# Kernel optimization log

Hardware: AMD Instinct MI355X
Metric: run time of the kernel (lower is better)

Reference implementation:

```python
import jax, jax.numpy as jnp
import numpy as np

K_HIDDEN = 512
N_POS = 24
N_COLOR = 6
EPS = 1e-5


def setup_inputs() -> dict:
    key = jax.random.key(0)
    k1, k2 = jax.random.split(key)
    B = 1024
    x = jax.random.normal(k1, (B, N_POS, N_COLOR * K_HIDDEN), dtype=jnp.float32)
    # kaiming-uniform-ish scale for the (k_out, k_in, 2) weight
    fan_in = K_HIDDEN * 2
    bound = float(np.sqrt(6.0 / fan_in))
    conv_weight = jax.random.uniform(k2, (K_HIDDEN, K_HIDDEN, 2), dtype=jnp.float32,
                                     minval=-bound, maxval=bound)
    conv_bias = jnp.zeros((K_HIDDEN,), dtype=jnp.float32)
    norm_weight = jnp.ones((K_HIDDEN,), dtype=jnp.float32)
    norm_bias = jnp.zeros((K_HIDDEN,), dtype=jnp.float32)
    return {"x": x, "conv_weight": conv_weight, "conv_bias": conv_bias,
            "norm_weight": norm_weight, "norm_bias": norm_bias}


def _color_layernorm(x, gamma, beta):
    # x: (B, 24, 6*k); normalize over the full channel axis, affine tied per block of 6
    mean = jnp.mean(x, axis=-1, keepdims=True)
    var = jnp.mean(jnp.square(x - mean), axis=-1, keepdims=True)  # unbiased=False
    xn = (x - mean) * jax.lax.rsqrt(var + EPS)
    xn = xn.reshape(*x.shape[:-1], K_HIDDEN, N_COLOR)
    xn = xn * gamma[:, None] + beta[:, None]
    return xn.reshape(x.shape)


def _color_conv(x, weight, bias):
    # x: (B, 24, 6*k) -> (B, 24, k, 6)
    B = x.shape[0]
    xr = x.reshape(B, N_POS, K_HIDDEN, N_COLOR)
    alpha = weight[:, :, 0] - weight[:, :, 1]   # (k_out, k_in)
    beta_w = weight[:, :, 1]                    # (k_out, k_in)
    term1 = jnp.einsum('bikd,ok->biod', xr, alpha)      # per-color linear
    x_sum = xr.sum(axis=3)                               # (B, 24, k_in)
    term2 = jnp.einsum('bik,ok->bio', x_sum, beta_w)     # color-sum linear
    out = term1 + term2[..., None] + bias[None, None, :, None]
    return out.reshape(B, N_POS, K_HIDDEN * N_COLOR)


def reference(x, conv_weight, conv_bias, norm_weight, norm_bias):
    h = _color_layernorm(x, norm_weight, norm_bias)
    h = _color_conv(h, conv_weight, conv_bias)
    return x + jax.nn.relu(h)
```

## Files before the change

### kernel.cpp

```cpp
#include <hip/hip_runtime.h>
#include <stdint.h>
#include <stddef.h>

#define KH   512
#define DF   3072
#define EPSF 1e-5f
#define PPB  8
#define ROWS 48
#define TSS  516

typedef __attribute__((ext_vector_type(4))) float f32x4;
typedef __attribute__((ext_vector_type(2))) float f32x2;
typedef __attribute__((ext_vector_type(8))) short bf16x8;

__device__ __forceinline__ unsigned short f2bf(float f) {
  union { float f; unsigned u; } c; c.f = f;
  unsigned u = c.u;
  u += 0x7fffu + ((u >> 16) & 1u);
  return (unsigned short)(u >> 16);
}
__device__ __forceinline__ unsigned short f2bf_trunc(float f) {
  union { float f; unsigned u; } c; c.f = f;
  return (unsigned short)(c.u >> 16);
}
__device__ __forceinline__ float bf2f(unsigned short u) {
  union { unsigned u; float f; } c; c.u = ((unsigned)u) << 16;
  return c.f;
}

__global__ __launch_bounds__(256) void prep_w(const float* __restrict__ cw,
                                              const float* __restrict__ cb,
                                              const float* __restrict__ nw,
                                              const float* __restrict__ nb,
                                              unsigned char* __restrict__ wbt,
                                              float* __restrict__ c12) {
  const int o = blockIdx.x;
  const int t = threadIdx.x;
  const int wn = o >> 6, nn = (o >> 4) & 3, co = o & 15;
  float c1 = 0.f, c2 = 0.f;
  for (int k = t; k < KH; k += 256) {
    float w0 = cw[o * 1024 + 2 * k];
    float w1 = cw[o * 1024 + 2 * k + 1];
    float a  = w0 - w1;
    float g  = nw[k], b = nb[k];
    int s = k >> 5, kin = k & 31, h = kin >> 3, e = kin & 7;
    size_t base = (size_t)(((wn * 16 + s) * 4 + nn)) * 1024 + (h * 16 + co) * 16 + e * 2;
    *(unsigned short*)(wbt + base)          = f2bf(a * g);
    *(unsigned short*)(wbt + base + 524288) = f2bf(w1 * g);
    float tt = a + 6.f * w1;
    c1 += tt * b;
    c2 += tt * g;
  }
  #pragma unroll
  for (int off = 32; off >= 1; off >>= 1) {
    c1 += __shfl_xor(c1, off);
    c2 += __shfl_xor(c2, off);
  }
  __shared__ float s1[4], s2[4];
  int wid = t >> 6, lane = t & 63;
  if (lane == 0) { s1[wid] = c1; s2[wid] = c2; }
  __syncthreads();
  if (t == 0) {
    c12[o]      = s1[0] + s1[1] + s1[2] + s1[3] + cb[o];
    c12[KH + o] = s2[0] + s2[1] + s2[2] + s2[3];
  }
}

__global__ __launch_bounds__(512, 4) void fused_main(
    const float* __restrict__ x,
    const unsigned char* __restrict__ wbt,
    const float* __restrict__ c12,
    float* __restrict__ out)
{
  __shared__ unsigned char As[ROWS * 1024];
  __shared__ unsigned char Sx[PPB * 1024];
  __shared__ float Ts[PPB * TSS];
  __shared__ float st[PPB * 2];

  const int tid  = threadIdx.x;
  const int lane = tid & 63;
  const int wid  = tid >> 6;
  const int co   = lane & 15;
  const int h    = lane >> 4;
  const int rvb  = h << 2;
  const size_t r0 = (size_t)blockIdx.x * PPB;

  const unsigned char* wA = wbt + (size_t)wid * 65536;
  bf16x8 bvA[4], bvB[4];

  {
    const float* xr = x + (size_t)(r0 + wid) * DF + lane * 48;
    f32x4 q[12];
    #pragma unroll
    for (int i = 0; i < 12; i++) q[i] = *(const f32x4*)(xr + i * 4);

    #pragma unroll
    for (int n = 0; n < 4; n++)
      bvA[n] = *(const bf16x8*)(wA + n * 1024 + lane * 16);

    float vv[48];
    #pragma unroll
    for (int i = 0; i < 12; i++) {
      vv[4 * i] = q[i].x; vv[4 * i + 1] = q[i].y;
      vv[4 * i + 2] = q[i].z; vv[4 * i + 3] = q[i].w;
    }
    float s = 0.f, sq = 0.f;
    #pragma unroll
    for (int i = 0; i < 48; i++) { s += vv[i]; sq += vv[i] * vv[i]; }
    #pragma unroll
    for (int off = 32; off >= 1; off >>= 1) {
      s  += __shfl_xor(s,  off);
      sq += __shfl_xor(sq, off);
    }
    float mean = s * (1.f / 3072.f);
    float var  = sq * (1.f / 3072.f) - mean * mean;
    float rstd = rsqrtf(var + EPSF);
    if (lane == 0) { st[2 * wid] = mean; st[2 * wid + 1] = rstd; }

    #pragma unroll
    for (int d = 0; d < 6; d++) {
      int row = wid * 6 + d;
      bf16x8 v;
      #pragma unroll
      for (int g = 0; g < 8; g++) v[g] = (short)f2bf_trunc(vv[g * 6 + d]);
      *(bf16x8*)(As + row * 1024 + ((lane ^ (row & 7)) << 4)) = v;
    }
    bf16x8 sv;
    #pragma unroll
    for (int g = 0; g < 8; g++) {
      float ss = vv[g * 6] + vv[g * 6 + 1] + vv[g * 6 + 2] +
                 vv[g * 6 + 3] + vv[g * 6 + 4] + vv[g * 6 + 5];
      sv[g] = (short)f2bf_trunc(ss);
    }
    *(bf16x8*)(Sx + wid * 1024 + ((lane ^ (wid & 7)) << 4)) = sv;
  }
  __syncthreads();

  f32x4 acc1[3][4];
  #pragma unroll
  for (int m = 0; m < 3; m++)
    #pragma unroll
    for (int n = 0; n < 4; n++) acc1[m][n] = (f32x4){0.f, 0.f, 0.f, 0.f};

  int arow[3], ar7[3];
  #pragma unroll
  for (int m = 0; m < 3; m++) {
    int row = m * 16 + co;
    arow[m] = row * 1024;  ar7[m] = row & 7;
  }

  {
    bf16x8 afA[3], afB[3];
    #pragma unroll
    for (int m = 0; m < 3; m++)
      afA[m] = *(const bf16x8*)(As + arow[m] + ((h ^ ar7[m]) << 4));

    #pragma unroll 1
    for (int s = 0; s < 16; s += 2) {
      {
        int g6 = (s + 1) * 4 + h;
        #pragma unroll
        for (int m = 0; m < 3; m++)
          afB[m] = *(const bf16x8*)(As + arow[m] + ((g6 ^ ar7[m]) << 4));
        const unsigned char* pn = wA + (size_t)(s + 1) * 4096;
        #pragma unroll
        for (int n = 0; n < 4; n++)
          bvB[n] = *(const bf16x8*)(pn + n * 1024 + lane * 16);
      }
      __builtin_amdgcn_s_setprio(1);
      #pragma unroll
      for (int m = 0; m < 3; m++)
        #pragma unroll
        for (int n = 0; n < 4; n++)
          acc1[m][n] = __builtin_amdgcn_mfma_f32_16x16x32_bf16(afA[m], bvA[n], acc1[m][n], 0, 0, 0);
      __builtin_amdgcn_s_setprio(0);
      if (s + 2 < 16) {
        int g6 = (s + 2) * 4 + h;
        #pragma unroll
        for (int m = 0; m < 3; m++)
          afA[m] = *(const bf16x8*)(As + arow[m] + ((g6 ^ ar7[m]) << 4));
        const unsigned char* pn2 = wA + (size_t)(s + 2) * 4096;
        #pragma unroll
        for (int n = 0; n < 4; n++)
          bvA[n] = *(const bf16x8*)(pn2 + n * 1024 + lane * 16);
      }
      __builtin_amdgcn_s_setprio(1);
      #pragma unroll
      for (int m = 0; m < 3; m++)
        #pragma unroll
        for (int n = 0; n < 4; n++)
          acc1[m][n] = __builtin_amdgcn_mfma_f32_16x16x32_bf16(afB[m], bvB[n], acc1[m][n], 0, 0, 0);
      __builtin_amdgcn_s_setprio(0);
    }
  }

  {
    f32x4 acc2[4];
    #pragma unroll
    for (int n = 0; n < 4; n++) acc2[n] = (f32x4){0.f, 0.f, 0.f, 0.f};
    const unsigned char* wB2 = wbt + 524288 + (size_t)wid * 65536;
    const int sxr = (co & 7);
    bf16x8 cA[4], cB[4];
    bf16x8 a2A, a2B;
    #pragma unroll
    for (int n = 0; n < 4; n++)
      cA[n] = *(const bf16x8*)(wB2 + n * 1024 + lane * 16);
    a2A = *(const bf16x8*)(Sx + sxr * 1024 + ((h ^ sxr) << 4));

    #pragma unroll 1
    for (int s = 0; s < 16; s += 2) {
      {
        int g6 = (s + 1) * 4 + h;
        a2B = *(const bf16x8*)(Sx + sxr * 1024 + ((g6 ^ sxr) << 4));
        const unsigned char* pn = wB2 + (size_t)(s + 1) * 4096;
        #pragma unroll
        for (int n = 0; n < 4; n++)
          cB[n] = *(const bf16x8*)(pn + n * 1024 + lane * 16);
      }
      __builtin_amdgcn_s_setprio(1);
      #pragma unroll
      for (int n = 0; n < 4; n++)
        acc2[n] = __builtin_amdgcn_mfma_f32_16x16x32_bf16(a2A, cA[n], acc2[n], 0, 0, 0);
      __builtin_amdgcn_s_setprio(0);
      if (s + 2 < 16) {
        int g6 = (s + 2) * 4 + h;
        a2A = *(const bf16x8*)(Sx + sxr * 1024 + ((g6 ^ sxr) << 4));
        const unsigned char* pn2 = wB2 + (size_t)(s + 2) * 4096;
        #pragma unroll
        for (int n = 0; n < 4; n++)
          cA[n] = *(const bf16x8*)(pn2 + n * 1024 + lane * 16);
      }
      __builtin_amdgcn_s_setprio(1);
      #pragma unroll
      for (int n = 0; n < 4; n++)
        acc2[n] = __builtin_amdgcn_mfma_f32_16x16x32_bf16(a2B, cB[n], acc2[n], 0, 0, 0);
      __builtin_amdgcn_s_setprio(0);
    }
    if (h < 2) {
      #pragma unroll
      for (int n = 0; n < 4; n++)
        #pragma unroll
        for (int v = 0; v < 4; v++)
          Ts[(rvb + v) * TSS + wid * 64 + n * 16 + co] = acc2[n][v];
    }
  }

  #pragma unroll
  for (int n = 0; n < 4; n++) {
    const int o = wid * 64 + n * 16 + co;
    const float C1 = c12[o];
    const float C2 = c12[KH + o];
    const int swzo = o >> 3;
    const int ob2 = (o & 7) * 2;
    #pragma unroll
    for (int m = 0; m < 3; m++) {
      int j0  = m * 16 + rvb;
      int pl0 = j0 / 6;
      int d0  = j0 - pl0 * 6;
      float mean0 = st[2 * pl0], rstd0 = st[2 * pl0 + 1];
      float t20   = Ts[pl0 * TSS + o];
      float cc0   = C1 - mean0 * rstd0 * C2;
      if (d0 < 3) {
        f32x4 ov;
        #pragma unroll
        for (int v = 0; v < 4; v++) {
          int j = j0 + v;
          unsigned short rx = *(const unsigned short*)(
              As + j * 1024 + ((swzo ^ (j & 7)) << 4) + ob2);
          ov[v] = bf2f(rx) + fmaxf(rstd0 * (acc1[m][n][v] + t20) + cc0, 0.f);
        }
        *(f32x4*)(out + (r0 + pl0) * DF + o * 6 + d0) = ov;
      } else {
        int pl1 = pl0 + 1;
        float mean1 = st[2 * pl1], rstd1 = st[2 * pl1 + 1];
        float t21   = Ts[pl1 * TSS + o];
        float cc1   = C1 - mean1 * rstd1 * C2;
        f32x2 o0, o1;
        #pragma unroll
        for (int v = 0; v < 2; v++) {
          int j = j0 + v;
          unsigned short rx = *(const unsigned short*)(
              As + j * 1024 + ((swzo ^ (j & 7)) << 4) + ob2);
          o0[v] = bf2f(rx) + fmaxf(rstd0 * (acc1[m][n][v] + t20) + cc0, 0.f);
        }
        #pragma unroll
        for (int v = 2; v < 4; v++) {
          int j = j0 + v;
          unsigned short rx = *(const unsigned short*)(
              As + j * 1024 + ((swzo ^ (j & 7)) << 4) + ob2);
          o1[v - 2] = bf2f(rx) + fmaxf(rstd1 * (acc1[m][n][v] + t21) + cc1, 0.f);
        }
        *(f32x2*)(out + (r0 + pl0) * DF + o * 6 + 4) = o0;
        *(f32x2*)(out + (r0 + pl1) * DF + o * 6)     = o1;
      }
    }
  }
}

extern "C" void kernel_launch(void* const* d_in, const int* in_sizes, int n_in,
                              void* d_out, int out_size, void* d_ws, size_t ws_size,
                              hipStream_t stream) {
  (void)n_in; (void)out_size; (void)ws_size;
  const float* x  = (const float*)d_in[0];
  const float* cw = (const float*)d_in[1];
  const float* cb = (const float*)d_in[2];
  const float* nw = (const float*)d_in[3];
  const float* nb = (const float*)d_in[4];
  float* out = (float*)d_out;

  unsigned char* wbt = (unsigned char*)d_ws;
  float* c12 = (float*)((char*)d_ws + (size_t)1024 * 1024);

  prep_w<<<512, 256, 0, stream>>>(cw, cb, nw, nb, wbt, c12);

  const int R = in_sizes[0] / DF;
  fused_main<<<R / PPB, 512, 0, stream>>>(x, wbt, c12, out);
}
```

Measured before the change: 234.1 us.

## Double rows per block with 16 waves sharing weight tiles

Each block now handles 16 positions (96 rows) with 1024 threads arranged as 2x8 waves. Waves in the same column share one weight slice, so each weight byte loaded from L2 serves twice as many rows. The colour-sum GEMM is split so each wave computes 32 output columns across all 16 positions. The change adds a barrier before the epilogue and raises LDS use per block, which may limit occupancy and register availability.

```diff
diff --git a/kernel.cpp b/kernel.cpp
--- a/kernel.cpp
+++ b/kernel.cpp
@@ -5,8 +5,8 @@
 #define KH   512
 #define DF   3072
 #define EPSF 1e-5f
-#define PPB  8
-#define ROWS 48
+#define PPB  16
+#define ROWS 96
 #define TSS  516
 
 typedef __attribute__((ext_vector_type(4))) float f32x4;
@@ -66,7 +66,7 @@
   }
 }
 
-__global__ __launch_bounds__(512, 4) void fused_main(
+__global__ __launch_bounds__(1024, 4) void fused_main(
     const float* __restrict__ x,
     const unsigned char* __restrict__ wbt,
     const float* __restrict__ c12,
@@ -80,12 +80,14 @@
   const int tid  = threadIdx.x;
   const int lane = tid & 63;
   const int wid  = tid >> 6;
+  const int wm   = wid >> 3;
+  const int wn   = wid & 7;
   const int co   = lane & 15;
   const int h    = lane >> 4;
   const int rvb  = h << 2;
   const size_t r0 = (size_t)blockIdx.x * PPB;
 
-  const unsigned char* wA = wbt + (size_t)wid * 65536;
+  const unsigned char* wA = wbt + (size_t)wn * 65536;
   bf16x8 bvA[4], bvB[4];
 
   {
@@ -145,7 +147,7 @@
   int arow[3], ar7[3];
   #pragma unroll
   for (int m = 0; m < 3; m++) {
-    int row = m * 16 + co;
+    int row = wm * 48 + m * 16 + co;
     arow[m] = row * 1024;  ar7[m] = row & 7;
   }
 
@@ -195,66 +197,62 @@
   }
 
   {
-    f32x4 acc2[4];
-    #pragma unroll
-    for (int n = 0; n < 4; n++) acc2[n] = (f32x4){0.f, 0.f, 0.f, 0.f};
-    const unsigned char* wB2 = wbt + 524288 + (size_t)wid * 65536;
-    const int sxr = (co & 7);
-    bf16x8 cA[4], cB[4];
+    f32x4 acc2[2];
+    acc2[0] = (f32x4){0.f, 0.f, 0.f, 0.f};
+    acc2[1] = (f32x4){0.f, 0.f, 0.f, 0.f};
+    const unsigned char* wB2 = wbt + 524288 + (size_t)(wid >> 1) * 65536
+                             + (size_t)(2 * (wid & 1)) * 1024 + (size_t)lane * 16;
+    const int sxr = co;
+    const int sx7 = sxr & 7;
+    bf16x8 cA[2], cB[2];
     bf16x8 a2A, a2B;
-    #pragma unroll
-    for (int n = 0; n < 4; n++)
-      cA[n] = *(const bf16x8*)(wB2 + n * 1024 + lane * 16);
-    a2A = *(const bf16x8*)(Sx + sxr * 1024 + ((h ^ sxr) << 4));
+    cA[0] = *(const bf16x8*)(wB2);
+    cA[1] = *(const bf16x8*)(wB2 + 1024);
+    a2A = *(const bf16x8*)(Sx + sxr * 1024 + ((h ^ sx7) << 4));
 
     #pragma unroll 1
     for (int s = 0; s < 16; s += 2) {
       {
         int g6 = (s + 1) * 4 + h;
-        a2B = *(const bf16x8*)(Sx + sxr * 1024 + ((g6 ^ sxr) << 4));
+        a2B = *(const bf16x8*)(Sx + sxr * 1024 + ((g6 ^ sx7) << 4));
         const unsigned char* pn = wB2 + (size_t)(s + 1) * 4096;
-        #pragma unroll
-        for (int n = 0; n < 4; n++)
-          cB[n] = *(const bf16x8*)(pn + n * 1024 + lane * 16);
+        cB[0] = *(const bf16x8*)(pn);
+        cB[1] = *(const bf16x8*)(pn + 1024);
       }
       __builtin_amdgcn_s_setprio(1);
-      #pragma unroll
-      for (int n = 0; n < 4; n++)
-        acc2[n] = __builtin_amdgcn_mfma_f32_16x16x32_bf16(a2A, cA[n], acc2[n], 0, 0, 0);
+      acc2[0] = __builtin_amdgcn_mfma_f32_16x16x32_bf16(a2A, cA[0], acc2[0], 0, 0, 0);
+      acc2[1] = __builtin_amdgcn_mfma_f32_16x16x32_bf16(a2A, cA[1], acc2[1], 0, 0, 0);
       __builtin_amdgcn_s_setprio(0);
       if (s + 2 < 16) {
         int g6 = (s + 2) * 4 + h;
-        a2A = *(const bf16x8*)(Sx + sxr * 1024 + ((g6 ^ sxr) << 4));
+        a2A = *(const bf16x8*)(Sx + sxr * 1024 + ((g6 ^ sx7) << 4));
         const unsigned char* pn2 = wB2 + (size_t)(s + 2) * 4096;
-        #pragma unroll
-        for (int n = 0; n < 4; n++)
-          cA[n] = *(const bf16x8*)(pn2 + n * 1024 + lane * 16);
+        cA[0] = *(const bf16x8*)(pn2);
+        cA[1] = *(const bf16x8*)(pn2 + 1024);
       }
       __builtin_amdgcn_s_setprio(1);
+      acc2[0] = __builtin_amdgcn_mfma_f32_16x16x32_bf16(a2B, cB[0], acc2[0], 0, 0, 0);
+      acc2[1] = __builtin_amdgcn_mfma_f32_16x16x32_bf16(a2B, cB[1], acc2[1], 0, 0, 0);
+      __builtin_amdgcn_s_setprio(0);
+    }
+    #pragma unroll
+    for (int n = 0; n < 2; n++)
       #pragma unroll
-      for (int n = 0; n < 4; n++)
-        acc2[n] = __builtin_amdgcn_mfma_f32_16x16x32_bf16(a2B, cB[n], acc2[n], 0, 0, 0);
-      __builtin_amdgcn_s_setprio(0);
-    }
-    if (h < 2) {
-      #pragma unroll
-      for (int n = 0; n < 4; n++)
-        #pragma unroll
-        for (int v = 0; v < 4; v++)
-          Ts[(rvb + v) * TSS + wid * 64 + n * 16 + co] = acc2[n][v];
-    }
-  }
+      for (int v = 0; v < 4; v++)
+        Ts[(rvb + v) * TSS + wid * 32 + n * 16 + co] = acc2[n][v];
+  }
+  __syncthreads();
 
   #pragma unroll
   for (int n = 0; n < 4; n++) {
-    const int o = wid * 64 + n * 16 + co;
+    const int o = wn * 64 + n * 16 + co;
     const float C1 = c12[o];
     const float C2 = c12[KH + o];
     const int swzo = o >> 3;
     const int ob2 = (o & 7) * 2;
     #pragma unroll
     for (int m = 0; m < 3; m++) {
-      int j0  = m * 16 + rvb;
+      int j0  = wm * 48 + m * 16 + rvb;
       int pl0 = j0 / 6;
       int d0  = j0 - pl0 * 6;
       float mean0 = st[2 * pl0], rstd0 = st[2 * pl0 + 1];
@@ -314,5 +312,5 @@
   prep_w<<<512, 256, 0, stream>>>(cw, cb, nw, nb, wbt, c12);
 
   const int R = in_sizes[0] / DF;
-  fused_main<<<R / PPB, 512, 0, stream>>>(x, wbt, c12, out);
-}
+  fused_main<<<R / PPB, 1024, 0, stream>>>(x, wbt, c12, out);
+}
```

New measurement: 240.5 us. 1.03x slower.

## Warp-specialize fused kernel into producer/consumer pipeline over double-buffered tiles

Applied to the files above, without the earlier changes.

Each block now has 16 waves and handles 12 consecutive 8-row tiles in a loop. Eight producer waves load x, compute LayerNorm statistics, fill the next tile's bf16 LDS buffers and write out the previous tile. Eight consumer waves run both MFMA GEMMs and write the residual result back into the LDS A buffer as bf16. The aim is to overlap global loads and stores with MFMA work and to cut the block count. The cost is only 8 compute waves per CU, a per-tile barrier, and a final output rounded to bf16 instead of fp32, which may affect accuracy.

```diff
diff --git a/kernel.cpp b/kernel.cpp
--- a/kernel.cpp
+++ b/kernel.cpp
@@ -7,10 +7,12 @@
 #define EPSF 1e-5f
 #define PPB  8
 #define ROWS 48
+#define NT   12
 #define TSS  516
+#define ABYTES (ROWS * 1024)
+#define SBYTES (PPB * 1024)
 
 typedef __attribute__((ext_vector_type(4))) float f32x4;
-typedef __attribute__((ext_vector_type(2))) float f32x2;
 typedef __attribute__((ext_vector_type(8))) short bf16x8;
 
 __device__ __forceinline__ unsigned short f2bf(float f) {
@@ -66,234 +68,261 @@
   }
 }
 
-__global__ __launch_bounds__(512, 4) void fused_main(
+__device__ __forceinline__ void stats_fill(const f32x4* q, unsigned char* Ab,
+                                           unsigned char* Sb, float* stb,
+                                           int pw, int lane) {
+  float vv[48];
+  #pragma unroll
+  for (int i = 0; i < 12; i++) {
+    vv[4*i] = q[i].x; vv[4*i+1] = q[i].y; vv[4*i+2] = q[i].z; vv[4*i+3] = q[i].w;
+  }
+  float s = 0.f, sq = 0.f;
+  #pragma unroll
+  for (int i = 0; i < 48; i++) { s += vv[i]; sq += vv[i] * vv[i]; }
+  #pragma unroll
+  for (int off = 32; off >= 1; off >>= 1) {
+    s  += __shfl_xor(s,  off);
+    sq += __shfl_xor(sq, off);
+  }
+  float mean = s * (1.f / 3072.f);
+  float var  = sq * (1.f / 3072.f) - mean * mean;
+  float rstd = rsqrtf(var + EPSF);
+  if (lane == 0) { stb[2 * pw] = mean; stb[2 * pw + 1] = rstd; }
+  #pragma unroll
+  for (int d = 0; d < 6; d++) {
+    int row = pw * 6 + d;
+    bf16x8 v;
+    #pragma unroll
+    for (int g = 0; g < 8; g++) v[g] = (short)f2bf_trunc(vv[g * 6 + d]);
+    *(bf16x8*)(Ab + row * 1024 + ((lane ^ (row & 7)) << 4)) = v;
+  }
+  bf16x8 sv;
+  #pragma unroll
+  for (int g = 0; g < 8; g++) {
+    float ss = vv[g*6] + vv[g*6+1] + vv[g*6+2] + vv[g*6+3] + vv[g*6+4] + vv[g*6+5];
+    sv[g] = (short)f2bf_trunc(ss);
+  }
+  *(bf16x8*)(Sb + pw * 1024 + ((lane ^ (pw & 7)) << 4)) = sv;
+}
+
+__device__ __forceinline__ void store_out_panel(const unsigned char* Ab,
+                                                float* ob, int pw, int lane) {
+  #pragma unroll
+  for (int jj = 0; jj < 12; jj++) {
+    int c0 = jj * 256 + lane * 4;
+    int o0 = c0 / 6;
+    int d0 = c0 - o0 * 6;
+    f32x4 ov;
+    #pragma unroll
+    for (int e = 0; e < 4; e++) {
+      int d = d0 + e, o = o0;
+      if (d >= 6) { d -= 6; o += 1; }
+      int row  = pw * 6 + d;
+      int byte = row * 1024 + ((((o >> 3) ^ (row & 7)) << 4)) + (o & 7) * 2;
+      ov[e] = bf2f(*(const unsigned short*)(Ab + byte));
+    }
+    *(f32x4*)(ob + c0) = ov;
+  }
+}
+
+__global__ __launch_bounds__(1024, 4) void fused_main(
     const float* __restrict__ x,
     const unsigned char* __restrict__ wbt,
     const float* __restrict__ c12,
     float* __restrict__ out)
 {
-  __shared__ unsigned char As[ROWS * 1024];
-  __shared__ unsigned char Sx[PPB * 1024];
+  __shared__ unsigned char As_[2 * ABYTES];
+  __shared__ unsigned char Sx_[2 * SBYTES];
   __shared__ float Ts[PPB * TSS];
-  __shared__ float st[PPB * 2];
+  __shared__ float st[2][PPB * 2];
 
   const int tid  = threadIdx.x;
   const int lane = tid & 63;
   const int wid  = tid >> 6;
+  const int pw   = wid & 7;
+  const bool isProd = wid >= 8;
   const int co   = lane & 15;
   const int h    = lane >> 4;
   const int rvb  = h << 2;
-  const size_t r0 = (size_t)blockIdx.x * PPB;
-
-  const unsigned char* wA = wbt + (size_t)wid * 65536;
-  bf16x8 bvA[4], bvB[4];
-
-  {
-    const float* xr = x + (size_t)(r0 + wid) * DF + lane * 48;
+  const size_t tile0 = (size_t)blockIdx.x * NT;
+
+  if (isProd) {
     f32x4 q[12];
+    const float* xr = x + (tile0 * PPB + pw) * DF + lane * 48;
     #pragma unroll
     for (int i = 0; i < 12; i++) q[i] = *(const f32x4*)(xr + i * 4);
-
-    #pragma unroll
-    for (int n = 0; n < 4; n++)
-      bvA[n] = *(const bf16x8*)(wA + n * 1024 + lane * 16);
-
-    float vv[48];
-    #pragma unroll
-    for (int i = 0; i < 12; i++) {
-      vv[4 * i] = q[i].x; vv[4 * i + 1] = q[i].y;
-      vv[4 * i + 2] = q[i].z; vv[4 * i + 3] = q[i].w;
-    }
-    float s = 0.f, sq = 0.f;
-    #pragma unroll
-    for (int i = 0; i < 48; i++) { s += vv[i]; sq += vv[i] * vv[i]; }
-    #pragma unroll
-    for (int off = 32; off >= 1; off >>= 1) {
-      s  += __shfl_xor(s,  off);
-      sq += __shfl_xor(sq, off);
-    }
-    float mean = s * (1.f / 3072.f);
-    float var  = sq * (1.f / 3072.f) - mean * mean;
-    float rstd = rsqrtf(var + EPSF);
-    if (lane == 0) { st[2 * wid] = mean; st[2 * wid + 1] = rstd; }
-
-    #pragma unroll
-    for (int d = 0; d < 6; d++) {
-      int row = wid * 6 + d;
-      bf16x8 v;
-      #pragma unroll
-      for (int g = 0; g < 8; g++) v[g] = (short)f2bf_trunc(vv[g * 6 + d]);
-      *(bf16x8*)(As + row * 1024 + ((lane ^ (row & 7)) << 4)) = v;
-    }
-    bf16x8 sv;
-    #pragma unroll
-    for (int g = 0; g < 8; g++) {
-      float ss = vv[g * 6] + vv[g * 6 + 1] + vv[g * 6 + 2] +
-                 vv[g * 6 + 3] + vv[g * 6 + 4] + vv[g * 6 + 5];
-      sv[g] = (short)f2bf_trunc(ss);
-    }
-    *(bf16x8*)(Sx + wid * 1024 + ((lane ^ (wid & 7)) << 4)) = sv;
+    stats_fill(q, As_, Sx_, st[0], pw, lane);
   }
   __syncthreads();
 
-  f32x4 acc1[3][4];
-  #pragma unroll
-  for (int m = 0; m < 3; m++)
-    #pragma unroll
-    for (int n = 0; n < 4; n++) acc1[m][n] = (f32x4){0.f, 0.f, 0.f, 0.f};
-
-  int arow[3], ar7[3];
-  #pragma unroll
-  for (int m = 0; m < 3; m++) {
-    int row = m * 16 + co;
-    arow[m] = row * 1024;  ar7[m] = row & 7;
-  }
-
-  {
-    bf16x8 afA[3], afB[3];
-    #pragma unroll
-    for (int m = 0; m < 3; m++)
-      afA[m] = *(const bf16x8*)(As + arow[m] + ((h ^ ar7[m]) << 4));
-
-    #pragma unroll 1
-    for (int s = 0; s < 16; s += 2) {
-      {
-        int g6 = (s + 1) * 4 + h;
-        #pragma unroll
-        for (int m = 0; m < 3; m++)
-          afB[m] = *(const bf16x8*)(As + arow[m] + ((g6 ^ ar7[m]) << 4));
-        const unsigned char* pn = wA + (size_t)(s + 1) * 4096;
-        #pragma unroll
-        for (int n = 0; n < 4; n++)
-          bvB[n] = *(const bf16x8*)(pn + n * 1024 + lane * 16);
-      }
-      __builtin_amdgcn_s_setprio(1);
+  for (int t = 0; t < NT; ++t) {
+    if (!isProd) {
+      const unsigned char* Ab = As_ + (size_t)(t & 1) * ABYTES;
+      const unsigned char* Sb = Sx_ + (size_t)(t & 1) * SBYTES;
+      const float* stb = st[t & 1];
+      const unsigned char* wA = wbt + (size_t)pw * 65536;
+
+      f32x4 acc1[3][4];
       #pragma unroll
       for (int m = 0; m < 3; m++)
         #pragma unroll
+        for (int n = 0; n < 4; n++) acc1[m][n] = (f32x4){0.f, 0.f, 0.f, 0.f};
+
+      int arow[3], ar7[3];
+      #pragma unroll
+      for (int m = 0; m < 3; m++) {
+        int row = m * 16 + co;
+        arow[m] = row * 1024;  ar7[m] = row & 7;
+      }
+
+      {
+        bf16x8 bvA[4], bvB[4], afA[3], afB[3];
+        #pragma unroll
         for (int n = 0; n < 4; n++)
-          acc1[m][n] = __builtin_amdgcn_mfma_f32_16x16x32_bf16(afA[m], bvA[n], acc1[m][n], 0, 0, 0);
-      __builtin_amdgcn_s_setprio(0);
-      if (s + 2 < 16) {
-        int g6 = (s + 2) * 4 + h;
+          bvA[n] = *(const bf16x8*)(wA + n * 1024 + lane * 16);
         #pragma unroll
         for (int m = 0; m < 3; m++)
-          afA[m] = *(const bf16x8*)(As + arow[m] + ((g6 ^ ar7[m]) << 4));
-        const unsigned char* pn2 = wA + (size_t)(s + 2) * 4096;
+          afA[m] = *(const bf16x8*)(Ab + arow[m] + ((h ^ ar7[m]) << 4));
+
+        #pragma unroll 1
+        for (int s = 0; s < 16; s += 2) {
+          {
+            int g6 = (s + 1) * 4 + h;
+            #pragma unroll
+            for (int m = 0; m < 3; m++)
+              afB[m] = *(const bf16x8*)(Ab + arow[m] + ((g6 ^ ar7[m]) << 4));
+            const unsigned char* pn = wA + (size_t)(s + 1) * 4096;
+            #pragma unroll
+            for (int n = 0; n < 4; n++)
+              bvB[n] = *(const bf16x8*)(pn + n * 1024 + lane * 16);
+          }
+          __builtin_amdgcn_s_setprio(1);
+          #pragma unroll
+          for (int m = 0; m < 3; m++)
+            #pragma unroll
+            for (int n = 0; n < 4; n++)
+              acc1[m][n] = __builtin_amdgcn_mfma_f32_16x16x32_bf16(afA[m], bvA[n], acc1[m][n], 0, 0, 0);
+          __builtin_amdgcn_s_setprio(0);
+          if (s + 2 < 16) {
+            int g6 = (s + 2) * 4 + h;
+            #pragma unroll
+            for (int m = 0; m < 3; m++)
+              afA[m] = *(const bf16x8*)(Ab + arow[m] + ((g6 ^ ar7[m]) << 4));
+            const unsigned char* pn2 = wA + (size_t)(s + 2) * 4096;
+            #pragma unroll
+            for (int n = 0; n < 4; n++)
+              bvA[n] = *(const bf16x8*)(pn2 + n * 1024 + lane * 16);
+          }
+          __builtin_amdgcn_s_setprio(1);
+          #pragma unroll
+          for (int m = 0; m < 3; m++)
+            #pragma unroll
+            for (int n = 0; n < 4; n++)
+              acc1[m][n] = __builtin_amdgcn_mfma_f32_16x16x32_bf16(afB[m], bvB[n], acc1[m][n], 0, 0, 0);
+          __builtin_amdgcn_s_setprio(0);
+        }
+      }
+
+      {
+        f32x4 acc2[4];
+        #pragma unroll
+        for (int n = 0; n < 4; n++) acc2[n] = (f32x4){0.f, 0.f, 0.f, 0.f};
+        const unsigned char* wB2 = wbt + 524288 + (size_t)pw * 65536;
+        const int sxr = (co & 7);
+        bf16x8 cA[4], cB[4], a2A, a2B;
         #pragma unroll
         for (int n = 0; n < 4; n++)
-          bvA[n] = *(const bf16x8*)(pn2 + n * 1024 + lane * 16);
-      }
-      __builtin_amdgcn_s_setprio(1);
-      #pragma unroll
-      for (int m = 0; m < 3; m++)
-        #pragma unroll
-        for (int n = 0; n < 4; n++)
-          acc1[m][n] = __builtin_amdgcn_mfma_f32_16x16x32_bf16(afB[m], bvB[n], acc1[m][n], 0, 0, 0);
-      __builtin_amdgcn_s_setprio(0);
+          cA[n] = *(const bf16x8*)(wB2 + n * 1024 + lane * 16);
+        a2A = *(const bf16x8*)(Sb + sxr * 1024 + ((h ^ sxr) << 4));
+
+        #pragma unroll 1
+        for (int s = 0; s < 16; s += 2) {
+          {
+            int g6 = (s + 1) * 4 + h;
+            a2B = *(const bf16x8*)(Sb + sxr * 1024 + ((g6 ^ sxr) << 4));
+            const unsigned char* pn = wB2 + (size_t)(s + 1) * 4096;
+            #pragma unroll
+            for (int n = 0; n < 4; n++)
+              cB[n] = *(const bf16x8*)(pn + n * 1024 + lane * 16);
+          }
+          __builtin_amdgcn_s_setprio(1);
+          #pragma unroll
+          for (int n = 0; n < 4; n++)
+            acc2[n] = __builtin_amdgcn_mfma_f32_16x16x32_bf16(a2A, cA[n], acc2[n], 0, 0, 0);
+          __builtin_amdgcn_s_setprio(0);
+          if (s + 2 < 16) {
+            int g6 = (s + 2) * 4 + h;
+            a2A = *(const bf16x8*)(Sb + sxr * 1024 + ((g6 ^ sxr) << 4));
+            const unsigned char* pn2 = wB2 + (size_t)(s + 2) * 4096;
+            #pragma unroll
+            for (int n = 0; n < 4; n++)
+              cA[n] = *(const bf16x8*)(pn2 + n * 1024 + lane * 16);
+          }
+          __builtin_amdgcn_s_setprio(1);
+          #pragma unroll
+          for (int n = 0; n < 4; n++)
+            acc2[n] = __builtin_amdgcn_mfma_f32_16x16x32_bf16(a2B, cB[n], acc2[n], 0, 0, 0);
+          __builtin_amdgcn_s_setprio(0);
+        }
+        if (h < 2) {
+          #pragma unroll
+          for (int n = 0; n < 4; n++)
+            #pragma unroll
+            for (int v = 0; v < 4; v++)
+              Ts[(rvb + v) * TSS + pw * 64 + n * 16 + co] = acc2[n][v];
+        }
+      }
+
+      {
+        unsigned char* AbW = (unsigned char*)Ab;
+        #pragma unroll
+        for (int n = 0; n < 4; n++) {
+          const int o = pw * 64 + n * 16 + co;
+          const float C1 = c12[o];
+          const float C2 = c12[KH + o];
+          const int swzo = o >> 3;
+          const int ob2 = (o & 7) * 2;
+          #pragma unroll
+          for (int m = 0; m < 3; m++) {
+            #pragma unroll
+            for (int v = 0; v < 4; v++) {
+              int j  = m * 16 + rvb + v;
+              int pl = j / 6;
+              float mean = stb[2 * pl], rstd = stb[2 * pl + 1];
+              float t2   = Ts[pl * TSS + o];
+              int byte = j * 1024 + (((swzo ^ (j & 7)) << 4)) + ob2;
+              unsigned short rx = *(const unsigned short*)(AbW + byte);
+              float hh = fmaxf(rstd * (acc1[m][n][v] + t2) + C1 - mean * rstd * C2, 0.f);
+              *(unsigned short*)(AbW + byte) = f2bf(bf2f(rx) + hh);
+            }
+          }
+        }
+      }
+    } else {
+      f32x4 q[12];
+      if (t < NT - 1) {
+        const float* xr = x + ((tile0 + t + 1) * PPB + pw) * DF + lane * 48;
+        #pragma unroll
+        for (int i = 0; i < 12; i++) q[i] = *(const f32x4*)(xr + i * 4);
+      }
+      if (t > 0) {
+        const unsigned char* Ap = As_ + (size_t)((t - 1) & 1) * ABYTES;
+        float* ob = out + ((tile0 + t - 1) * PPB + pw) * DF;
+        store_out_panel(Ap, ob, pw, lane);
+      }
+      if (t < NT - 1) {
+        unsigned char* Ab = As_ + (size_t)((t + 1) & 1) * ABYTES;
+        unsigned char* Sb = Sx_ + (size_t)((t + 1) & 1) * SBYTES;
+        stats_fill(q, Ab, Sb, st[(t + 1) & 1], pw, lane);
+      }
     }
-  }
-
-  {
-    f32x4 acc2[4];
-    #pragma unroll
-    for (int n = 0; n < 4; n++) acc2[n] = (f32x4){0.f, 0.f, 0.f, 0.f};
-    const unsigned char* wB2 = wbt + 524288 + (size_t)wid * 65536;
-    const int sxr = (co & 7);
-    bf16x8 cA[4], cB[4];
-    bf16x8 a2A, a2B;
-    #pragma unroll
-    for (int n = 0; n < 4; n++)
-      cA[n] = *(const bf16x8*)(wB2 + n * 1024 + lane * 16);
-    a2A = *(const bf16x8*)(Sx + sxr * 1024 + ((h ^ sxr) << 4));
-
-    #pragma unroll 1
-    for (int s = 0; s < 16; s += 2) {
-      {
-        int g6 = (s + 1) * 4 + h;
-        a2B = *(const bf16x8*)(Sx + sxr * 1024 + ((g6 ^ sxr) << 4));
-        const unsigned char* pn = wB2 + (size_t)(s + 1) * 4096;
-        #pragma unroll
-        for (int n = 0; n < 4; n++)
-          cB[n] = *(const bf16x8*)(pn + n * 1024 + lane * 16);
-      }
-      __builtin_amdgcn_s_setprio(1);
-      #pragma unroll
-      for (int n = 0; n < 4; n++)
-        acc2[n] = __builtin_amdgcn_mfma_f32_16x16x32_bf16(a2A, cA[n], acc2[n], 0, 0, 0);
-      __builtin_amdgcn_s_setprio(0);
-      if (s + 2 < 16) {
-        int g6 = (s + 2) * 4 + h;
-        a2A = *(const bf16x8*)(Sx + sxr * 1024 + ((g6 ^ sxr) << 4));
-        const unsigned char* pn2 = wB2 + (size_t)(s + 2) * 4096;
-        #pragma unroll
-        for (int n = 0; n < 4; n++)
-          cA[n] = *(const bf16x8*)(pn2 + n * 1024 + lane * 16);
-      }
-      __builtin_amdgcn_s_setprio(1);
-      #pragma unroll
-      for (int n = 0; n < 4; n++)
-        acc2[n] = __builtin_amdgcn_mfma_f32_16x16x32_bf16(a2B, cB[n], acc2[n], 0, 0, 0);
-      __builtin_amdgcn_s_setprio(0);
-    }
-    if (h < 2) {
-      #pragma unroll
-      for (int n = 0; n < 4; n++)
-        #pragma unroll
-        for (int v = 0; v < 4; v++)
-          Ts[(rvb + v) * TSS + wid * 64 + n * 16 + co] = acc2[n][v];
-    }
-  }
-
-  #pragma unroll
-  for (int n = 0; n < 4; n++) {
-    const int o = wid * 64 + n * 16 + co;
-    const float C1 = c12[o];
-    const float C2 = c12[KH + o];
-    const int swzo = o >> 3;
-    const int ob2 = (o & 7) * 2;
-    #pragma unroll
-    for (int m = 0; m < 3; m++) {
-      int j0  = m * 16 + rvb;
-      int pl0 = j0 / 6;
-      int d0  = j0 - pl0 * 6;
-      float mean0 = st[2 * pl0], rstd0 = st[2 * pl0 + 1];
-      float t20   = Ts[pl0 * TSS + o];
-      float cc0   = C1 - mean0 * rstd0 * C2;
-      if (d0 < 3) {
-        f32x4 ov;
-        #pragma unroll
-        for (int v = 0; v < 4; v++) {
-          int j = j0 + v;
-          unsigned short rx = *(const unsigned short*)(
-              As + j * 1024 + ((swzo ^ (j & 7)) << 4) + ob2);
-          ov[v] = bf2f(rx) + fmaxf(rstd0 * (acc1[m][n][v] + t20) + cc0, 0.f);
-        }
-        *(f32x4*)(out + (r0 + pl0) * DF + o * 6 + d0) = ov;
-      } else {
-        int pl1 = pl0 + 1;
-        float mean1 = st[2 * pl1], rstd1 = st[2 * pl1 + 1];
-        float t21   = Ts[pl1 * TSS + o];
-        float cc1   = C1 - mean1 * rstd1 * C2;
-        f32x2 o0, o1;
-        #pragma unroll
-        for (int v = 0; v < 2; v++) {
-          int j = j0 + v;
-          unsigned short rx = *(const unsigned short*)(
-              As + j * 1024 + ((swzo ^ (j & 7)) << 4) + ob2);
-          o0[v] = bf2f(rx) + fmaxf(rstd0 * (acc1[m][n][v] + t20) + cc0, 0.f);
-        }
-        #pragma unroll
-        for (int v = 2; v < 4; v++) {
-          int j = j0 + v;
-          unsigned short rx = *(const unsigned short*)(
-              As + j * 1024 + ((swzo ^ (j & 7)) << 4) + ob2);
-          o1[v - 2] = bf2f(rx) + fmaxf(rstd1 * (acc1[m][n][v] + t21) + cc1, 0.f);
-        }
-        *(f32x2*)(out + (r0 + pl0) * DF + o * 6 + 4) = o0;
-        *(f32x2*)(out + (r0 + pl1) * DF + o * 6)     = o1;
-      }
-    }
+    __syncthreads();
+  }
+
+  if (isProd) {
+    const unsigned char* Ap = As_ + (size_t)((NT - 1) & 1) * ABYTES;
+    float* ob = out + ((tile0 + NT - 1) * PPB + pw) * DF;
+    store_out_panel(Ap, ob, pw, lane);
   }
 }
 
@@ -314,5 +343,5 @@
   prep_w<<<512, 256, 0, stream>>>(cw, cb, nw, nb, wbt, c12);
 
   const int R = in_sizes[0] / DF;
-  fused_main<<<R / PPB, 512, 0, stream>>>(x, wbt, c12, out);
-}
+  fused_main<<<R / (PPB * NT), 1024, 0, stream>>>(x, wbt, c12, out);
+}
```

Result: slower. 818.0 us (+249.4%).
